# Kernel optimization log

Measured on AMD Instinct MI355X. Metric: run time of the kernel, lower is better.

Reference implementation:

```python
import jax, jax.numpy as jnp
import numpy as np

EMBED_DIM = 1024
NUM_HEADS = 16
HEAD_DIM = EMBED_DIM // NUM_HEADS
GLOBAL_HEADS = 1
LOCAL_K = 128
SCALE = HEAD_DIM ** -0.5


def setup_inputs() -> dict:
    key = jax.random.key(0)
    ks = jax.random.split(key, 9)
    B, n = 4, 2048
    s = 1.0 / np.sqrt(EMBED_DIM)  # torch Linear default uniform(-1/sqrt(in), 1/sqrt(in))
    def lin(k):
        kw, kb = jax.random.split(k)
        W = jax.random.uniform(kw, (EMBED_DIM, EMBED_DIM), jnp.float32, -s, s)
        b = jax.random.uniform(kb, (EMBED_DIM,), jnp.float32, -s, s)
        return W, b
    wq, bq = lin(ks[0])
    wk, bk = lin(ks[1])
    wv, bv = lin(ks[2])
    wo, bo = lin(ks[3])
    x = jax.random.normal(ks[4], (B, n, EMBED_DIM), jnp.float32)
    return {"x": x, "wq": wq, "bq": bq, "wk": wk, "bk": bk,
            "wv": wv, "bv": bv, "wo": wo, "bo": bo}


def _attend(x, wq, bq, wk, bk, wv, bv, wo, bo):
    B, n, E = x.shape
    H, D = NUM_HEADS, HEAD_DIM
    def proj(W, b):
        t = x @ W.T + b                       # [B, n, E]
        return t.reshape(B, n, H, D).transpose(0, 2, 1, 3)  # [B, H, n, D]
    q, k, v = proj(wq, bq), proj(wk, bk), proj(wv, bv)
    scores = jnp.einsum('bhqd,bhkd->bhqk', q, k) * SCALE  # [B, H, n, n]
    idx = jnp.arange(n)
    band = jnp.abs(idx[:, None] - idx[None, :]) <= LOCAL_K  # [n, n] True = allowed
    is_global = jnp.arange(H) < GLOBAL_HEADS
    mask = band[None, :, :] | is_global[:, None, None]      # [H, n, n]
    scores = jnp.where(mask[None], scores, -jnp.inf)
    attn = jax.nn.softmax(scores, axis=-1)   # dropout is identity (p=0 / eval)
    out = jnp.einsum('bhqk,bhkd->bhqd', attn, v)
    out = out.transpose(0, 2, 1, 3).reshape(B, n, E)
    return out @ wo.T + bo


def reference(x, wq, bq, wk, bk, wv, bv, wo, bo):
    return _attend(x, wq, bq, wk, bk, wv, bv, wo, bo)
```

## Files before the change

kernel.cpp:

```cpp
#include <hip/hip_runtime.h>

typedef __attribute__((ext_vector_type(4))) float f32x4;
typedef __attribute__((ext_vector_type(8))) short s16x8;

#define GLDS(gsrc, ldst) \
  __builtin_amdgcn_global_load_lds((const __attribute__((address_space(1))) void*)(gsrc), \
                                   (__attribute__((address_space(3))) void*)(ldst), 16, 0, 0)

__device__ __forceinline__ ushort f2bf(float f) {
  union { float f; unsigned u; } x; x.f = f;
  unsigned r = (x.u + 0x7FFFu + ((x.u >> 16) & 1u)) >> 16;
  return (ushort)r;
}

__global__ __launch_bounds__(256) void castk(const float* __restrict__ in,
                                             ushort* __restrict__ outp, int n) {
  int i = (blockIdx.x * 256 + threadIdx.x) * 4;
  if (i >= n) return;
  float4 v = *(const float4*)(in + i);
  ushort4 r;
  r.x = f2bf(v.x); r.y = f2bf(v.y); r.z = f2bf(v.z); r.w = f2bf(v.w);
  *(ushort4*)(outp + i) = r;
}

__global__ __launch_bounds__(256) void castw(const float* __restrict__ w0, const float* __restrict__ w1,
                                             const float* __restrict__ w2, const float* __restrict__ w3,
                                             ushort* __restrict__ o0, ushort* __restrict__ o1,
                                             ushort* __restrict__ o2, ushort* __restrict__ o3) {
  int bid = blockIdx.x;
  int sel = bid >> 10;
  const float* in = (sel == 0) ? w0 : (sel == 1) ? w1 : (sel == 2) ? w2 : w3;
  ushort* outp    = (sel == 0) ? o0 : (sel == 1) ? o1 : (sel == 2) ? o2 : o3;
  int i = ((bid & 1023) * 256 + threadIdx.x) * 4;
  float4 v = *(const float4*)(in + i);
  ushort4 r;
  r.x = f2bf(v.x); r.y = f2bf(v.y); r.z = f2bf(v.z); r.w = f2bf(v.w);
  *(ushort4*)(outp + i) = r;
}

template<int OUTBF16>
__global__ __launch_bounds__(512, 2) void gemm256(
    const ushort* __restrict__ A, const ushort* __restrict__ Bt,
    const float* __restrict__ bias0, const float* __restrict__ bias1,
    const float* __restrict__ bias2,
    void* __restrict__ Cout, int M, int N, int K, int nxn)
{
  __shared__ __align__(16) ushort lds[73728];
  const int tid = threadIdx.x;
  const int w = tid >> 6, lane = tid & 63;
  const int lrow = lane & 15, lg = lane >> 4;
  const int wm = w >> 2, wn = w & 3;
  const int cpx = gridDim.x >> 3;
  const int wgid = ((int)blockIdx.x & 7) * cpx + ((int)blockIdx.x >> 3);
  const int mblk = (wgid / nxn) * 128;
  const int nblk = (wgid % nxn) * 256;
  const int NT = K >> 6;

  const int srow = tid >> 3;
  const int scol = 8 * ((tid & 7) ^ (srow & 7));
  const ushort* Abase = A + (size_t)(mblk + srow) * K + scol;
  const ushort* Bbase = Bt + (size_t)(nblk + srow) * K + scol;
  const size_t rstep = (size_t)64 * K;
  const int dA = w * 512;
  const int dB = 8192 + w * 512;

#define STAGE_A(p, bf) { \
    GLDS((p),         &lds[(bf) + dA]); \
    GLDS((p) + rstep, &lds[(bf) + dA + 4096]); }
#define STAGE_B(p, bf) { \
    GLDS((p),             &lds[(bf) + dB]); \
    GLDS((p) + rstep,     &lds[(bf) + dB + 4096]); \
    GLDS((p) + 2 * rstep, &lds[(bf) + dB + 8192]); \
    GLDS((p) + 3 * rstep, &lds[(bf) + dB + 12288]); }

  const int laneA0 = (wm * 64 + lrow) * 64 + ((lg ^ (lrow & 7)) << 3);
  const int laneA1 = (wm * 64 + lrow) * 64 + (((4 + lg) ^ (lrow & 7)) << 3);
  const int laneB0 = 8192 + (wn * 64 + lrow) * 64 + ((lg ^ (lrow & 7)) << 3);
  const int laneB1 = 8192 + (wn * 64 + lrow) * 64 + (((4 + lg) ^ (lrow & 7)) << 3);

  const f32x4 zero = {0.f, 0.f, 0.f, 0.f};
  f32x4 acc[4][4];
#pragma unroll
  for (int m = 0; m < 4; m++)
#pragma unroll
    for (int n = 0; n < 4; n++) acc[m][n] = zero;

  STAGE_A(Abase, 0); STAGE_B(Bbase, 0);
  if (NT > 1) { STAGE_A(Abase + 64, 24576); STAGE_B(Bbase + 64, 24576); }

  const ushort* aP = Abase + 128;
  const ushort* bP = Bbase + 128;
  int bb = 0, bbS = 49152;

  for (int t = 0; t < NT; ++t) {
    if (t < NT - 1) { asm volatile("s_waitcnt vmcnt(6)" ::: "memory"); }
    else            { asm volatile("s_waitcnt vmcnt(0)" ::: "memory"); }
    __builtin_amdgcn_s_barrier();
    const int pA0 = bb + laneA0, pA1 = bb + laneA1;
    const int pB0 = bb + laneB0, pB1 = bb + laneB1;
    const bool pf = (t + 2 < NT);

    if (pf) STAGE_A(aP, bbS);
    {
      s16x8 af[4], bf_[4];
#pragma unroll
      for (int m = 0; m < 4; m++) af[m] = *(const s16x8*)&lds[pA0 + m * 1024];
#pragma unroll
      for (int n = 0; n < 4; n++) bf_[n] = *(const s16x8*)&lds[pB0 + n * 1024];
      __builtin_amdgcn_s_setprio(1);
#pragma unroll
      for (int m = 0; m < 4; m++)
#pragma unroll
        for (int n = 0; n < 4; n++)
          acc[m][n] = __builtin_amdgcn_mfma_f32_16x16x32_bf16(af[m], bf_[n], acc[m][n], 0, 0, 0);
      __builtin_amdgcn_s_setprio(0);
    }
    if (pf) STAGE_B(bP, bbS);
    {
      s16x8 af[4], bf_[4];
#pragma unroll
      for (int m = 0; m < 4; m++) af[m] = *(const s16x8*)&lds[pA1 + m * 1024];
#pragma unroll
      for (int n = 0; n < 4; n++) bf_[n] = *(const s16x8*)&lds[pB1 + n * 1024];
      __builtin_amdgcn_s_setprio(1);
#pragma unroll
      for (int m = 0; m < 4; m++)
#pragma unroll
        for (int n = 0; n < 4; n++)
          acc[m][n] = __builtin_amdgcn_mfma_f32_16x16x32_bf16(af[m], bf_[n], acc[m][n], 0, 0, 0);
      __builtin_amdgcn_s_setprio(0);
    }
    if (pf) { aP += 64; bP += 64; }
    bb  = (bb  == 49152) ? 0 : bb + 24576;
    bbS = (bbS == 49152) ? 0 : bbS + 24576;
  }
#undef STAGE_A
#undef STAGE_B

  float bias_n[4];
#pragma unroll
  for (int n = 0; n < 4; n++) {
    const int col = nblk + wn * 64 + n * 16 + lrow;
    if (bias1) bias_n[n] = (col < 1024) ? bias0[col]
                          : (col < 2048 ? bias1[col - 1024] : bias2[col - 2048]);
    else bias_n[n] = bias0[col];
  }

  __syncthreads();

  if (OUTBF16) {
    ushort* Ct = lds;
#pragma unroll
    for (int m = 0; m < 4; m++)
#pragma unroll
      for (int n = 0; n < 4; n++)
#pragma unroll
        for (int i = 0; i < 4; i++)
          Ct[(wm * 64 + m * 16 + 4 * lg + i) * 256 + wn * 64 + n * 16 + lrow] =
              f2bf(acc[m][n][i] + bias_n[n]);
    __syncthreads();
    ushort* Cg = (ushort*)Cout;
#pragma unroll
    for (int r = 0; r < 8; r++) {
      const int row = r * 16 + (tid >> 5);
      const int col = (tid & 31) * 8;
      *(s16x8*)&Cg[(size_t)(mblk + row) * N + nblk + col] = *(const s16x8*)&lds[r * 4096 + tid * 8];
    }
  } else {
    float* Cf = (float*)lds;
#pragma unroll
    for (int m = 0; m < 4; m++)
#pragma unroll
      for (int n = 0; n < 4; n++)
#pragma unroll
        for (int i = 0; i < 4; i++)
          Cf[(wm * 64 + m * 16 + 4 * lg + i) * 256 + wn * 64 + n * 16 + lrow] =
              acc[m][n][i] + bias_n[n];
    __syncthreads();
    float* Cg = (float*)Cout;
#pragma unroll
    for (int r = 0; r < 16; r++) {
      const int row = r * 8 + (tid >> 6);
      const int col = (tid & 63) * 4;
      *(float4*)&Cg[(size_t)(mblk + row) * N + nblk + col] = *(const float4*)&Cf[r * 2048 + tid * 4];
    }
  }
}

__global__ __launch_bounds__(256) void attn_kernel(const ushort* __restrict__ qkv,
                                                   ushort* __restrict__ outp,
                                                   float* __restrict__ oPart,
                                                   float* __restrict__ mPart,
                                                   float* __restrict__ lPart)
{
  __shared__ __align__(16) ushort Ks[64 * 64];
  __shared__ __align__(16) ushort Vt[64 * 64];
  __shared__ __align__(16) ushort Ps[4][16 * 40];

  const int tid = threadIdx.x;
  const int w = tid >> 6, lane = tid & 63;
  const int lrow = lane & 15, lg = lane >> 4;

  const int bid = (blockIdx.x & 7) * 368 + (blockIdx.x >> 3);
  int h, b, bx, kv_lo, kv_hi, chunk = 0;
  bool isGlobal;
  if (bid < 1024) {
    isGlobal = true; h = 0;
    chunk = bid >> 7;
    int qb = bid & 127;
    b = qb >> 5; bx = qb & 31;
    kv_lo = chunk * 256; kv_hi = kv_lo + 256;
  } else {
    isGlobal = false;
    int t = bid - 1024;
    h = 1 + (t >> 7);
    int qb = t & 127;
    b = qb >> 5; bx = qb & 31;
    kv_lo = bx * 64 - 128; if (kv_lo < 0) kv_lo = 0;
    kv_hi = bx * 64 + 192; if (kv_hi > 2048) kv_hi = 2048;
  }
  const int q0b = bx * 64;
  const int q0 = q0b + w * 16;
  const ushort* Qp = qkv + (size_t)b * 2048 * 3072 + h * 64;
  const ushort* Kp = Qp + 1024;
  const ushort* Vp = Qp + 2048;

  s16x8 qf0 = *(const s16x8*)(Qp + (size_t)(q0 + lrow) * 3072 + 8 * lg);
  s16x8 qf1 = *(const s16x8*)(Qp + (size_t)(q0 + lrow) * 3072 + 32 + 8 * lg);

  const f32x4 zero = {0.f, 0.f, 0.f, 0.f};
  f32x4 o[4];
  o[0] = zero; o[1] = zero; o[2] = zero; o[3] = zero;
  float mrun = -3e38f, lsum = 0.f;
  const int q_abs = q0 + lrow;
  const float SCL = 0.18033688011112042f;

  const int sp = tid >> 3;
  const int sg = tid & 7;
  const int kr0 = tid >> 3;
  const int kc = tid & 7;
  const int vx = (lrow & 7) ^ (lrow >> 3);

  for (int kv = kv_lo; kv < kv_hi; kv += 64) {
    const bool needMask = !isGlobal && (kv < q0b - 64 || kv + 64 > q0b + 128);

    const ushort* vrow = Vp + (size_t)(kv + 2 * sp) * 3072 + 8 * sg;
    s16x8 vlo = *(const s16x8*)vrow;
    s16x8 vhi = *(const s16x8*)(vrow + 3072);

    __syncthreads();

    GLDS(Kp + (size_t)(kv + kr0) * 3072 + 8 * (kc ^ (kr0 & 7)), &Ks[w * 512]);
    GLDS(Kp + (size_t)(kv + 32 + kr0) * 3072 + 8 * (kc ^ (kr0 & 7)), &Ks[2048 + w * 512]);

#pragma unroll
    for (int j = 0; j < 8; j++) {
      const int d = 8 * sg + j;
      const int r = 2 * sp;
      uint pk = (uint)(ushort)vlo[j] | ((uint)(ushort)vhi[j] << 16);
      *(uint*)&Vt[d * 64 + ((((r >> 3) ^ j ^ sg) & 7) << 3) + (r & 7)] = pk;
    }
    __syncthreads();

#pragma unroll
    for (int s = 0; s < 2; s++) {
      const int kb = kv + 32 * s;
      const int rs = 32 * s;
      s16x8 kA0 = *(const s16x8*)&Ks[(rs + lrow) * 64      + ((( lg      ^ (lrow & 7)) & 7) << 3)];
      s16x8 kA1 = *(const s16x8*)&Ks[(rs + lrow) * 64      + ((((4 + lg) ^ (lrow & 7)) & 7) << 3)];
      s16x8 kB0 = *(const s16x8*)&Ks[(rs + 16 + lrow) * 64 + ((( lg      ^ (lrow & 7)) & 7) << 3)];
      s16x8 kB1 = *(const s16x8*)&Ks[(rs + 16 + lrow) * 64 + ((((4 + lg) ^ (lrow & 7)) & 7) << 3)];

      f32x4 sA = __builtin_amdgcn_mfma_f32_16x16x32_bf16(kA0, qf0, zero, 0, 0, 0);
      sA = __builtin_amdgcn_mfma_f32_16x16x32_bf16(kA1, qf1, sA, 0, 0, 0);
      f32x4 sB = __builtin_amdgcn_mfma_f32_16x16x32_bf16(kB0, qf0, zero, 0, 0, 0);
      sB = __builtin_amdgcn_mfma_f32_16x16x32_bf16(kB1, qf1, sB, 0, 0, 0);

      float pA[4], pB[4];
      float rowmax = -3e38f;
      if (needMask) {
#pragma unroll
        for (int i = 0; i < 4; i++) {
          int kaA = kb + 4 * lg + i;
          int dq = q_abs - kaA;
          float va = (dq <= 128 && dq >= -128) ? sA[i] * SCL : -1e30f;
          pA[i] = va; rowmax = fmaxf(rowmax, va);
          int dqb = dq - 16;
          float vb = (dqb <= 128 && dqb >= -128) ? sB[i] * SCL : -1e30f;
          pB[i] = vb; rowmax = fmaxf(rowmax, vb);
        }
      } else {
#pragma unroll
        for (int i = 0; i < 4; i++) {
          pA[i] = sA[i] * SCL; pB[i] = sB[i] * SCL;
          rowmax = fmaxf(rowmax, fmaxf(pA[i], pB[i]));
        }
      }
      rowmax = fmaxf(rowmax, __shfl_xor(rowmax, 16));
      rowmax = fmaxf(rowmax, __shfl_xor(rowmax, 32));

      if (!__all(rowmax <= mrun + 8.f)) {
        float mnew = fmaxf(mrun, rowmax);
        float alpha = exp2f(mrun - mnew);
        mrun = mnew;
        lsum *= alpha;
        float a0 = __shfl(alpha, 4 * lg + 0);
        float a1 = __shfl(alpha, 4 * lg + 1);
        float a2 = __shfl(alpha, 4 * lg + 2);
        float a3 = __shfl(alpha, 4 * lg + 3);
#pragma unroll
        for (int c = 0; c < 4; c++) {
          o[c][0] *= a0; o[c][1] *= a1; o[c][2] *= a2; o[c][3] *= a3;
        }
      }

      float rsum = 0.f;
      if (needMask) {
#pragma unroll
        for (int i = 0; i < 4; i++) {
          pA[i] = (pA[i] > -1e29f) ? exp2f(pA[i] - mrun) : 0.f;
          pB[i] = (pB[i] > -1e29f) ? exp2f(pB[i] - mrun) : 0.f;
          rsum += pA[i] + pB[i];
        }
      } else {
#pragma unroll
        for (int i = 0; i < 4; i++) {
          pA[i] = exp2f(pA[i] - mrun);
          pB[i] = exp2f(pB[i] - mrun);
          rsum += pA[i] + pB[i];
        }
      }
      rsum += __shfl_xor(rsum, 16);
      rsum += __shfl_xor(rsum, 32);
      lsum += rsum;

      {
        ushort* P = &Ps[w][lrow * 40];
        *(uint*)&P[4 * lg]      = (uint)f2bf(pA[0]) | ((uint)f2bf(pA[1]) << 16);
        *(uint*)&P[4 * lg + 2]  = (uint)f2bf(pA[2]) | ((uint)f2bf(pA[3]) << 16);
        *(uint*)&P[16 + 4 * lg] = (uint)f2bf(pB[0]) | ((uint)f2bf(pB[1]) << 16);
        *(uint*)&P[18 + 4 * lg] = (uint)f2bf(pB[2]) | ((uint)f2bf(pB[3]) << 16);
      }
      s16x8 paf = *(const s16x8*)&Ps[w][lrow * 40 + 8 * lg];

#pragma unroll
      for (int c = 0; c < 4; c++) {
        const int d = 16 * c + lrow;
        s16x8 vf = *(const s16x8*)&Vt[d * 64 + ((((4 * s + lg) ^ vx ^ (2 * c)) & 7) << 3)];
        o[c] = __builtin_amdgcn_mfma_f32_16x16x32_bf16(paf, vf, o[c], 0, 0, 0);
      }
    }
  }

  if (isGlobal) {
    const size_t rbase = (size_t)(chunk * 4 + b) * 2048 + q0;
    if (lg == 0) {
      mPart[rbase + lrow] = mrun;
      lPart[rbase + lrow] = lsum;
    }
#pragma unroll
    for (int c = 0; c < 4; c++)
#pragma unroll
      for (int i = 0; i < 4; i++)
        oPart[(rbase + 4 * lg + i) * 64 + 16 * c + lrow] = o[c][i];
  } else {
    float li0 = 1.f / __shfl(lsum, 4 * lg + 0);
    float li1 = 1.f / __shfl(lsum, 4 * lg + 1);
    float li2 = 1.f / __shfl(lsum, 4 * lg + 2);
    float li3 = 1.f / __shfl(lsum, 4 * lg + 3);
    size_t orow = (size_t)(b * 2048 + q0 + 4 * lg);
#pragma unroll
    for (int c = 0; c < 4; c++) {
      outp[(orow + 0) * 1024 + h * 64 + 16 * c + lrow] = f2bf(o[c][0] * li0);
      outp[(orow + 1) * 1024 + h * 64 + 16 * c + lrow] = f2bf(o[c][1] * li1);
      outp[(orow + 2) * 1024 + h * 64 + 16 * c + lrow] = f2bf(o[c][2] * li2);
      outp[(orow + 3) * 1024 + h * 64 + 16 * c + lrow] = f2bf(o[c][3] * li3);
    }
  }
}

__global__ __launch_bounds__(256) void combine_kernel(const float* __restrict__ oPart,
                                                      const float* __restrict__ mPart,
                                                      const float* __restrict__ lPart,
                                                      ushort* __restrict__ attno) {
  const int tid = threadIdx.x;
  const int row = blockIdx.x * 64 + (tid >> 2);
  const int d0 = (tid & 3) * 16;
  float m[8], l[8], M = -3e38f;
#pragma unroll
  for (int p = 0; p < 8; p++) {
    m[p] = mPart[p * 8192 + row];
    l[p] = lPart[p * 8192 + row];
    M = fmaxf(M, m[p]);
  }
  float L = 0.f, wgt[8];
#pragma unroll
  for (int p = 0; p < 8; p++) { wgt[p] = exp2f(m[p] - M); L += wgt[p] * l[p]; }
  float inv = 1.f / L;
  float acc[16];
#pragma unroll
  for (int j = 0; j < 16; j++) acc[j] = 0.f;
#pragma unroll
  for (int p = 0; p < 8; p++) {
    const float* op = oPart + ((size_t)p * 8192 + row) * 64 + d0;
    float wv = wgt[p];
#pragma unroll
    for (int j = 0; j < 16; j += 4) {
      float4 v = *(const float4*)(op + j);
      acc[j]     += wv * v.x; acc[j + 1] += wv * v.y;
      acc[j + 2] += wv * v.z; acc[j + 3] += wv * v.w;
    }
  }
  ushort* dst = attno + (size_t)row * 1024 + d0;
#pragma unroll
  for (int j = 0; j < 16; j++) dst[j] = f2bf(acc[j] * inv);
}

extern "C" void kernel_launch(void* const* d_in, const int* in_sizes, int n_in,
                              void* d_out, int out_size, void* d_ws, size_t ws_size,
                              hipStream_t stream) {
  const float* x  = (const float*)d_in[0];
  const float* wq = (const float*)d_in[1];
  const float* bq = (const float*)d_in[2];
  const float* wk = (const float*)d_in[3];
  const float* bk = (const float*)d_in[4];
  const float* wv = (const float*)d_in[5];
  const float* bv = (const float*)d_in[6];
  const float* wo = (const float*)d_in[7];
  const float* bo = (const float*)d_in[8];

  char* ws = (char*)d_ws;
  ushort* xb    = (ushort*)(ws);
  ushort* wqkvb = (ushort*)(ws + 16777216);
  ushort* wob   = (ushort*)(ws + 23068672);
  ushort* qkvb  = (ushort*)(ws + 25165824);
  ushort* attno = (ushort*)(ws + 75497472);
  float* oPart = (float*)(ws);
  float* mPart = (float*)(ws + 16777216);
  float* lPart = (float*)(ws + 16777216 + 262144);

  castk<<<8192, 256, 0, stream>>>(x, xb, 8388608);
  castw<<<4096, 256, 0, stream>>>(wq, wk, wv, wo,
                                  wqkvb, wqkvb + 1048576, wqkvb + 2097152, wob);

  gemm256<1><<<768, 512, 0, stream>>>(xb, wqkvb, bq, bk, bv,
                                      (void*)qkvb, 8192, 3072, 1024, 12);

  attn_kernel<<<2944, 256, 0, stream>>>(qkvb, attno, oPart, mPart, lPart);
  combine_kernel<<<128, 256, 0, stream>>>(oPart, mPart, lPart, attno);

  gemm256<0><<<256, 512, 0, stream>>>(attno, wob, bo, nullptr, nullptr,
                                      (void*)d_out, 8192, 1024, 1024, 4);
}
```

Measured before the change: 165.6 us.

## Double-buffer K/V tiles in attention and merge cast kernels into one launch

The attention loop now keeps two LDS buffers for K and V. The next tile's K is issued via global_load_lds and its V is loaded into registers while the current tile is being computed, with one barrier per iteration instead of two. This hides global memory latency behind MFMA work, at the cost of doubled LDS use per block and hand-written waitcnt logic. Separately, the x cast and the weight cast kernels are merged into a single launch to save one kernel dispatch.

```diff
diff --git a/kernel.cpp b/kernel.cpp
--- a/kernel.cpp
+++ b/kernel.cpp
@@ -13,29 +13,22 @@
   return (ushort)r;
 }
 
-__global__ __launch_bounds__(256) void castk(const float* __restrict__ in,
-                                             ushort* __restrict__ outp, int n) {
-  int i = (blockIdx.x * 256 + threadIdx.x) * 4;
-  if (i >= n) return;
+__global__ __launch_bounds__(256) void castall(
+    const float* __restrict__ x, const float* __restrict__ wq, const float* __restrict__ wk,
+    const float* __restrict__ wv, const float* __restrict__ wo,
+    ushort* __restrict__ xb, ushort* __restrict__ wqkvb, ushort* __restrict__ wob) {
+  int bid = blockIdx.x;
+  const float* in; ushort* op;
+  if (bid < 8192)       { in = x;  op = xb; }
+  else if (bid < 9216)  { in = wq; op = wqkvb;           bid -= 8192; }
+  else if (bid < 10240) { in = wk; op = wqkvb + 1048576; bid -= 9216; }
+  else if (bid < 11264) { in = wv; op = wqkvb + 2097152; bid -= 10240; }
+  else                  { in = wo; op = wob;             bid -= 11264; }
+  int i = (bid * 256 + threadIdx.x) * 4;
   float4 v = *(const float4*)(in + i);
   ushort4 r;
   r.x = f2bf(v.x); r.y = f2bf(v.y); r.z = f2bf(v.z); r.w = f2bf(v.w);
-  *(ushort4*)(outp + i) = r;
-}
-
-__global__ __launch_bounds__(256) void castw(const float* __restrict__ w0, const float* __restrict__ w1,
-                                             const float* __restrict__ w2, const float* __restrict__ w3,
-                                             ushort* __restrict__ o0, ushort* __restrict__ o1,
-                                             ushort* __restrict__ o2, ushort* __restrict__ o3) {
-  int bid = blockIdx.x;
-  int sel = bid >> 10;
-  const float* in = (sel == 0) ? w0 : (sel == 1) ? w1 : (sel == 2) ? w2 : w3;
-  ushort* outp    = (sel == 0) ? o0 : (sel == 1) ? o1 : (sel == 2) ? o2 : o3;
-  int i = ((bid & 1023) * 256 + threadIdx.x) * 4;
-  float4 v = *(const float4*)(in + i);
-  ushort4 r;
-  r.x = f2bf(v.x); r.y = f2bf(v.y); r.z = f2bf(v.z); r.w = f2bf(v.w);
-  *(ushort4*)(outp + i) = r;
+  *(ushort4*)(op + i) = r;
 }
 
 template<int OUTBF16>
@@ -193,8 +186,8 @@
                                                    float* __restrict__ mPart,
                                                    float* __restrict__ lPart)
 {
-  __shared__ __align__(16) ushort Ks[64 * 64];
-  __shared__ __align__(16) ushort Vt[64 * 64];
+  __shared__ __align__(16) ushort Ks[2][64 * 64];
+  __shared__ __align__(16) ushort Vt[2][64 * 64];
   __shared__ __align__(16) ushort Ps[4][16 * 40];
 
   const int tid = threadIdx.x;
@@ -241,35 +234,48 @@
   const int kc = tid & 7;
   const int vx = (lrow & 7) ^ (lrow >> 3);
 
+  const ushort* vr0 = Vp + (size_t)(kv_lo + 2 * sp) * 3072 + 8 * sg;
+  s16x8 vlo = *(const s16x8*)vr0;
+  s16x8 vhi = *(const s16x8*)(vr0 + 3072);
+  GLDS(Kp + (size_t)(kv_lo + kr0) * 3072 + 8 * (kc ^ (kr0 & 7)), &Ks[0][w * 512]);
+  GLDS(Kp + (size_t)(kv_lo + 32 + kr0) * 3072 + 8 * (kc ^ (kr0 & 7)), &Ks[0][2048 + w * 512]);
+
+  int buf = 0;
   for (int kv = kv_lo; kv < kv_hi; kv += 64) {
     const bool needMask = !isGlobal && (kv < q0b - 64 || kv + 64 > q0b + 128);
-
-    const ushort* vrow = Vp + (size_t)(kv + 2 * sp) * 3072 + 8 * sg;
-    s16x8 vlo = *(const s16x8*)vrow;
-    s16x8 vhi = *(const s16x8*)(vrow + 3072);
-
-    __syncthreads();
-
-    GLDS(Kp + (size_t)(kv + kr0) * 3072 + 8 * (kc ^ (kr0 & 7)), &Ks[w * 512]);
-    GLDS(Kp + (size_t)(kv + 32 + kr0) * 3072 + 8 * (kc ^ (kr0 & 7)), &Ks[2048 + w * 512]);
+    const bool hasNext = (kv + 64 < kv_hi);
+
+    s16x8 vlon, vhin;
+    if (hasNext) {
+      const ushort* vr = Vp + (size_t)(kv + 64 + 2 * sp) * 3072 + 8 * sg;
+      vlon = *(const s16x8*)vr;
+      vhin = *(const s16x8*)(vr + 3072);
+    }
 
 #pragma unroll
     for (int j = 0; j < 8; j++) {
       const int d = 8 * sg + j;
       const int r = 2 * sp;
       uint pk = (uint)(ushort)vlo[j] | ((uint)(ushort)vhi[j] << 16);
-      *(uint*)&Vt[d * 64 + ((((r >> 3) ^ j ^ sg) & 7) << 3) + (r & 7)] = pk;
-    }
-    __syncthreads();
+      *(uint*)&Vt[buf][d * 64 + ((((r >> 3) ^ j ^ sg) & 7) << 3) + (r & 7)] = pk;
+    }
+    if (hasNext) asm volatile("s_waitcnt vmcnt(2)" ::: "memory");
+    else         asm volatile("s_waitcnt vmcnt(0)" ::: "memory");
+    asm volatile("s_waitcnt lgkmcnt(0)" ::: "memory");
+    __builtin_amdgcn_s_barrier();
+    if (hasNext) {
+      GLDS(Kp + (size_t)(kv + 64 + kr0) * 3072 + 8 * (kc ^ (kr0 & 7)), &Ks[buf ^ 1][w * 512]);
+      GLDS(Kp + (size_t)(kv + 96 + kr0) * 3072 + 8 * (kc ^ (kr0 & 7)), &Ks[buf ^ 1][2048 + w * 512]);
+    }
 
 #pragma unroll
     for (int s = 0; s < 2; s++) {
       const int kb = kv + 32 * s;
       const int rs = 32 * s;
-      s16x8 kA0 = *(const s16x8*)&Ks[(rs + lrow) * 64      + ((( lg      ^ (lrow & 7)) & 7) << 3)];
-      s16x8 kA1 = *(const s16x8*)&Ks[(rs + lrow) * 64      + ((((4 + lg) ^ (lrow & 7)) & 7) << 3)];
-      s16x8 kB0 = *(const s16x8*)&Ks[(rs + 16 + lrow) * 64 + ((( lg      ^ (lrow & 7)) & 7) << 3)];
-      s16x8 kB1 = *(const s16x8*)&Ks[(rs + 16 + lrow) * 64 + ((((4 + lg) ^ (lrow & 7)) & 7) << 3)];
+      s16x8 kA0 = *(const s16x8*)&Ks[buf][(rs + lrow) * 64      + ((( lg      ^ (lrow & 7)) & 7) << 3)];
+      s16x8 kA1 = *(const s16x8*)&Ks[buf][(rs + lrow) * 64      + ((((4 + lg) ^ (lrow & 7)) & 7) << 3)];
+      s16x8 kB0 = *(const s16x8*)&Ks[buf][(rs + 16 + lrow) * 64 + ((( lg      ^ (lrow & 7)) & 7) << 3)];
+      s16x8 kB1 = *(const s16x8*)&Ks[buf][(rs + 16 + lrow) * 64 + ((((4 + lg) ^ (lrow & 7)) & 7) << 3)];
 
       f32x4 sA = __builtin_amdgcn_mfma_f32_16x16x32_bf16(kA0, qf0, zero, 0, 0, 0);
       sA = __builtin_amdgcn_mfma_f32_16x16x32_bf16(kA1, qf1, sA, 0, 0, 0);
@@ -346,10 +352,13 @@
 #pragma unroll
       for (int c = 0; c < 4; c++) {
         const int d = 16 * c + lrow;
-        s16x8 vf = *(const s16x8*)&Vt[d * 64 + ((((4 * s + lg) ^ vx ^ (2 * c)) & 7) << 3)];
+        s16x8 vf = *(const s16x8*)&Vt[buf][d * 64 + ((((4 * s + lg) ^ vx ^ (2 * c)) & 7) << 3)];
         o[c] = __builtin_amdgcn_mfma_f32_16x16x32_bf16(paf, vf, o[c], 0, 0, 0);
       }
     }
+
+    vlo = vlon; vhi = vhin;
+    buf ^= 1;
   }
 
   if (isGlobal) {
@@ -439,9 +448,7 @@
   float* mPart = (float*)(ws + 16777216);
   float* lPart = (float*)(ws + 16777216 + 262144);
 
-  castk<<<8192, 256, 0, stream>>>(x, xb, 8388608);
-  castw<<<4096, 256, 0, stream>>>(wq, wk, wv, wo,
-                                  wqkvb, wqkvb + 1048576, wqkvb + 2097152, wob);
+  castall<<<12288, 256, 0, stream>>>(x, wq, wk, wv, wo, xb, wqkvb, wob);
 
   gemm256<1><<<768, 512, 0, stream>>>(xb, wqkvb, bq, bk, bv,
                                       (void*)qkvb, 8192, 3072, 1024, 12);
```

Result: slower. 172.4 us (+4.1%).
